# Performance work log

Measured on AMD Instinct MI355X. Metric: run time of the kernel, lower is better.

Reference implementation:

```python
import jax, jax.numpy as jnp
import numpy as np

D_MODEL = 14
N_HEADS = 2
SINK_TEMP = 0.1
SINK_ITERS = 20
EPS = 1e-10


def setup_inputs() -> dict:
    key = jax.random.key(0)
    ks = jax.random.split(key, 12)
    b, n, d = 64, 1024, D_MODEL
    s = 1.0 / np.sqrt(d)
    return {
        "x": jax.random.normal(ks[0], (b, n, d), dtype=jnp.float32),
        "certainty": jax.random.uniform(ks[1], (b, n), dtype=jnp.float32),
        "permutation": jax.random.randint(ks[2], (b, n), 0, n).astype(jnp.int64),
        "Wq": jax.random.normal(ks[3], (d, d), dtype=jnp.float32) * s,
        "bq": jnp.zeros((d,), dtype=jnp.float32),
        "Wk": jax.random.normal(ks[4], (d, d), dtype=jnp.float32) * s,
        "bk": jnp.zeros((d,), dtype=jnp.float32),
        "Wv": jax.random.normal(ks[5], (d, d), dtype=jnp.float32) * s,
        "bv": jnp.zeros((d,), dtype=jnp.float32),
        "Wo": jax.random.normal(ks[6], (d, d), dtype=jnp.float32) * s,
        "bo": jnp.zeros((d,), dtype=jnp.float32),
    }


def _split_heads(t, b, n):
    # (b, n, d) -> (b, H, n, hd)
    return t.reshape(b, n, N_HEADS, D_MODEL // N_HEADS).transpose(0, 2, 1, 3)


def reference(x, certainty, permutation, Wq, bq, Wk, bk, Wv, bv, Wo, bo):
    b, n, d = x.shape
    hd = d // N_HEADS
    Q = _split_heads(x @ Wq.T + bq, b, n)
    K = _split_heads(x @ Wk.T + bk, b, n)
    V = _split_heads(x @ Wv.T + bv, b, n)
    scores = jnp.einsum("bhqd,bhkd->bhqk", Q, K) / jnp.sqrt(jnp.float32(hd))
    attn = jax.nn.softmax(scores, axis=-1)  # dropout is identity at eval
    out = jnp.einsum("bhqk,bhkd->bhqd", attn, V)
    out = out.transpose(0, 2, 1, 3).reshape(b, n, d)
    out = out @ Wo.T + bo

    avg_attn = attn.mean(axis=1)  # (b, n, n)
    entropy = -jnp.sum(avg_attn * jnp.log(avg_attn + EPS), axis=-1)  # (b, n)
    max_entropy = jnp.log(jnp.float32(n))
    cert_update = jax.nn.sigmoid(max_entropy - entropy)
    new_certainty = jnp.maximum(certainty, cert_update)

    logits = jnp.log(avg_attn + EPS)
    P = jnp.exp(logits / SINK_TEMP)

    def body(_, P):
        P = P / (P.sum(axis=-1, keepdims=True) + EPS)
        P = P / (P.sum(axis=-2, keepdims=True) + EPS)
        return P

    P = jax.lax.fori_loop(0, SINK_ITERS, body, P)
    new_perm = jnp.argmax(P, axis=-1)  # (b, n)
    new_permutation = jnp.take_along_axis(permutation, new_perm, axis=1)
    return out, new_certainty, new_permutation
```

## Files before the change

### kernel.cpp

```cpp
#include <hip/hip_runtime.h>

#define EPSF    1e-10f
#define MAXENT  6.93147180559945286f
#define SCALEF  0.37796447300922720f

__device__ __forceinline__ float wave_sum(float v) {
#pragma unroll
  for (int off = 32; off > 0; off >>= 1) v += __shfl_xor(v, off);
  return v;
}
__device__ __forceinline__ void wave_sum2(float& a, float& b) {
#pragma unroll
  for (int off = 32; off > 0; off >>= 1) {
    a += __shfl_xor(a, off);
    b += __shfl_xor(b, off);
  }
}
__device__ __forceinline__ void fma4(float a, float4 b, float4& c) {
  c.x = fmaf(a, b.x, c.x); c.y = fmaf(a, b.y, c.y);
  c.z = fmaf(a, b.z, c.z); c.w = fmaf(a, b.w, c.w);
}
__device__ __forceinline__ float dot4(float4 a, float4 b, float acc) {
  acc = fmaf(a.x, b.x, acc); acc = fmaf(a.y, b.y, acc);
  acc = fmaf(a.z, b.z, acc); acc = fmaf(a.w, b.w, acc);
  return acc;
}
__device__ __forceinline__ float4 exp4(float4 s) {
  return make_float4(__expf(s.x), __expf(s.y), __expf(s.z), __expf(s.w));
}
__device__ __forceinline__ float p0e(float s1, float s2, float E1, float E2) {
  float p = fmaf(E1, __expf(s1), fmaf(E2, __expf(s2), EPSF));
  float p2 = p * p, p4 = p2 * p2, p5 = p4 * p;
  return p5 * p5;
}

__global__ __launch_bounds__(256) void qkv_kernel(
    const float* __restrict__ x,
    const float* __restrict__ Wq, const float* __restrict__ bq,
    const float* __restrict__ Wk, const float* __restrict__ bk,
    const float* __restrict__ Wv, const float* __restrict__ bv,
    float* __restrict__ Qt, float* __restrict__ Kt, float* __restrict__ Vt,
    float* __restrict__ R, float* __restrict__ CA, float* __restrict__ CB) {
  int row = blockIdx.x * 256 + threadIdx.x;
  int b = row >> 10, i = row & 1023;
  float xv[14];
#pragma unroll
  for (int k = 0; k < 14; k++) xv[k] = x[row * 14 + k];
#pragma unroll
  for (int d = 0; d < 14; d++) {
    float q = bq[d], kk = bk[d], vv = bv[d];
#pragma unroll
    for (int k = 0; k < 14; k++) {
      q  = fmaf(xv[k], Wq[d * 14 + k], q);
      kk = fmaf(xv[k], Wk[d * 14 + k], kk);
      vv = fmaf(xv[k], Wv[d * 14 + k], vv);
    }
    int o = b * 14336 + d * 1024 + i;
    Qt[o] = q * SCALEF;
    Kt[o] = kk; Vt[o] = vv;
  }
  R[row] = 1.0f;
  CA[row] = 1.0f;
  CB[row] = 1.0f;
}

__global__ __launch_bounds__(256, 2) void attn_kernel(
    const float* __restrict__ Qt, const float* __restrict__ Kt, const float* __restrict__ Vt,
    const float* __restrict__ cert_in,
    const float* __restrict__ WoG, const float* __restrict__ boG,
    float* __restrict__ E1o, float* __restrict__ E2o,
    float* __restrict__ out_, float* __restrict__ cert_out) {
  __shared__ float4 Kl[3584];
  __shared__ float WoS[196];
  __shared__ float boS[14];
  int b = blockIdx.x >> 7;
  int rg = blockIdx.x & 127;
  int tid = threadIdx.x;
  const float4* Ktb = (const float4*)(Kt + b * 14336);
  for (int idx = tid; idx < 3584; idx += 256) Kl[idx] = Ktb[idx];
  if (tid < 196) WoS[tid] = WoG[tid];
  if (tid < 14) boS[tid] = boG[tid];
  __syncthreads();

  int wave = tid >> 6, lane = tid & 63;
  int i0 = rg * 8 + wave * 2;
  float q0[14], q1[14];
#pragma unroll
  for (int d = 0; d < 14; d++) {
    q0[d] = Qt[b * 14336 + d * 1024 + i0];
    q1[d] = Qt[b * 14336 + d * 1024 + i0 + 1];
  }

  float4 e10[4], e20[4], e11[4], e21[4];
  float L10 = 0.f, L20 = 0.f, L11 = 0.f, L21 = 0.f;
  float acc0[14], acc1[14];
#pragma unroll
  for (int d = 0; d < 14; d++) { acc0[d] = 0.f; acc1[d] = 0.f; }
  const float4* Vtb = (const float4*)(Vt + b * 14336);
#pragma unroll
  for (int t = 0; t < 4; t++) {
    int g = t * 64 + lane;
    float4 kv[7];
#pragma unroll
    for (int d = 0; d < 7; d++) kv[d] = Kl[d * 256 + g];
    float4 sa = {0,0,0,0}, sb = {0,0,0,0};
#pragma unroll
    for (int d = 0; d < 7; d++) { fma4(q0[d], kv[d], sa); fma4(q1[d], kv[d], sb); }
    e10[t] = exp4(sa); e11[t] = exp4(sb);
    L10 += e10[t].x + e10[t].y + e10[t].z + e10[t].w;
    L11 += e11[t].x + e11[t].y + e11[t].z + e11[t].w;
#pragma unroll
    for (int d = 0; d < 7; d++) kv[d] = Kl[(d + 7) * 256 + g];
    sa = make_float4(0,0,0,0); sb = make_float4(0,0,0,0);
#pragma unroll
    for (int d = 0; d < 7; d++) { fma4(q0[d + 7], kv[d], sa); fma4(q1[d + 7], kv[d], sb); }
    e20[t] = exp4(sa); e21[t] = exp4(sb);
    L20 += e20[t].x + e20[t].y + e20[t].z + e20[t].w;
    L21 += e21[t].x + e21[t].y + e21[t].z + e21[t].w;
#pragma unroll
    for (int d = 0; d < 7; d++) {
      float4 vv = Vtb[d * 256 + g];
      acc0[d] += e10[t].x * vv.x + e10[t].y * vv.y + e10[t].z * vv.z + e10[t].w * vv.w;
      acc1[d] += e11[t].x * vv.x + e11[t].y * vv.y + e11[t].z * vv.z + e11[t].w * vv.w;
    }
#pragma unroll
    for (int d = 7; d < 14; d++) {
      float4 vv = Vtb[d * 256 + g];
      acc0[d] += e20[t].x * vv.x + e20[t].y * vv.y + e20[t].z * vv.z + e20[t].w * vv.w;
      acc1[d] += e21[t].x * vv.x + e21[t].y * vv.y + e21[t].z * vv.z + e21[t].w * vv.w;
    }
  }
  wave_sum2(L10, L20); wave_sum2(L11, L21);
  float i10 = 1.0f / L10, i20 = 1.0f / L20, i11 = 1.0f / L11, i21 = 1.0f / L21;

  float ent0 = 0.f, ent1 = 0.f;
#pragma unroll
  for (int t = 0; t < 4; t++) {
    float a;
    a = 0.5f * (e10[t].x * i10 + e20[t].x * i20); ent0 -= a * __logf(a + EPSF);
    a = 0.5f * (e10[t].y * i10 + e20[t].y * i20); ent0 -= a * __logf(a + EPSF);
    a = 0.5f * (e10[t].z * i10 + e20[t].z * i20); ent0 -= a * __logf(a + EPSF);
    a = 0.5f * (e10[t].w * i10 + e20[t].w * i20); ent0 -= a * __logf(a + EPSF);
    a = 0.5f * (e11[t].x * i11 + e21[t].x * i21); ent1 -= a * __logf(a + EPSF);
    a = 0.5f * (e11[t].y * i11 + e21[t].y * i21); ent1 -= a * __logf(a + EPSF);
    a = 0.5f * (e11[t].z * i11 + e21[t].z * i21); ent1 -= a * __logf(a + EPSF);
    a = 0.5f * (e11[t].w * i11 + e21[t].w * i21); ent1 -= a * __logf(a + EPSF);
  }
  wave_sum2(ent0, ent1);
#pragma unroll
  for (int d = 0; d < 14; d += 2) wave_sum2(acc0[d], acc0[d + 1]);
#pragma unroll
  for (int d = 0; d < 14; d += 2) wave_sum2(acc1[d], acc1[d + 1]);

  int row0 = b * 1024 + i0;
  if (lane == 0) {
    E1o[row0] = 0.5f * i10;  E2o[row0] = 0.5f * i20;
    E1o[row0 + 1] = 0.5f * i11; E2o[row0 + 1] = 0.5f * i21;
    cert_out[row0] = fmaxf(cert_in[row0], 1.0f / (1.0f + __expf(ent0 - MAXENT)));
    cert_out[row0 + 1] = fmaxf(cert_in[row0 + 1], 1.0f / (1.0f + __expf(ent1 - MAXENT)));
  }
  if (lane < 14) {
    int d = lane;
    float av0[14], av1[14];
#pragma unroll
    for (int k = 0; k < 14; k++) {
      av0[k] = acc0[k] * (k < 7 ? i10 : i20);
      av1[k] = acc1[k] * (k < 7 ? i11 : i21);
    }
    float s0 = boS[d], s1 = boS[d];
#pragma unroll
    for (int k = 0; k < 14; k++) {
      s0 = fmaf(av0[k], WoS[d * 14 + k], s0);
      s1 = fmaf(av1[k], WoS[d * 14 + k], s1);
    }
    out_[(size_t)row0 * 14 + d] = s0;
    out_[(size_t)(row0 + 1) * 14 + d] = s1;
  }
}


__global__ __launch_bounds__(512) void p0sink1_kernel(
    const float* __restrict__ Qt, const float* __restrict__ Kt,
    const float* __restrict__ E1, const float* __restrict__ E2,
    float* __restrict__ P0, float* __restrict__ R,
    float* __restrict__ vpart, int b0, int G) {
  __shared__ float4 Kl[3584];
  int gb = blockIdx.x >> 5, blk = blockIdx.x & 31;
  int b = b0 + gb;
  int tid = threadIdx.x;
  const float4* Ktb = (const float4*)(Kt + b * 14336);
  for (int idx = tid; idx < 3584; idx += 512) Kl[idx] = Ktb[idx];
  __syncthreads();

  int wave = tid >> 6, lane = tid & 63;
  int i0 = blk * 32 + wave * 4;
  float q[4][14], e1r[4], e2r[4], u[4];
#pragma unroll
  for (int rr = 0; rr < 4; rr++) {
#pragma unroll
    for (int d = 0; d < 14; d++) q[rr][d] = Qt[b * 14336 + d * 1024 + i0 + rr];
    e1r[rr] = E1[b * 1024 + i0 + rr];
    e2r[rr] = E2[b * 1024 + i0 + rr];
    u[rr] = 0.f;
  }
  float4* P0f4 = (float4*)P0;
#pragma unroll
  for (int t = 0; t < 4; t++) {
    int g = t * 64 + lane;
    float4 kv[14];
#pragma unroll
    for (int d = 0; d < 14; d++) kv[d] = Kl[d * 256 + g];
#pragma unroll
    for (int rr = 0; rr < 4; rr++) {
      float4 s1 = {0,0,0,0}, s2 = {0,0,0,0};
#pragma unroll
      for (int d = 0; d < 7; d++)  fma4(q[rr][d], kv[d], s1);
#pragma unroll
      for (int d = 7; d < 14; d++) fma4(q[rr][d], kv[d], s2);
      float4 pv;
      pv.x = p0e(s1.x, s2.x, e1r[rr], e2r[rr]);
      pv.y = p0e(s1.y, s2.y, e1r[rr], e2r[rr]);
      pv.z = p0e(s1.z, s2.z, e1r[rr], e2r[rr]);
      pv.w = p0e(s1.w, s2.w, e1r[rr], e2r[rr]);
      P0f4[(size_t)(gb * 1024 + i0 + rr) * 256 + g] = pv;
      u[rr] += pv.x; u[rr] += pv.y; u[rr] += pv.z; u[rr] += pv.w;
    }
  }
  wave_sum2(u[0], u[1]); wave_sum2(u[2], u[3]);
  float rv[4];
#pragma unroll
  for (int rr = 0; rr < 4; rr++) {
    float r0 = 1.0f;
    rv[rr] = fminf(r0 / fmaf(r0, u[rr], EPSF), 1e37f);
  }
  if (lane == 0) {
#pragma unroll
    for (int rr = 0; rr < 4; rr++) R[b * 1024 + i0 + rr] = rv[rr];
  }
  int l0 = lane, l1 = 64 + lane, l2 = 128 + lane, l3 = 192 + lane;
  float4 v0 = {0,0,0,0}, v1 = {0,0,0,0}, v2 = {0,0,0,0}, v3 = {0,0,0,0};
  const float4* base = P0f4 + (size_t)(gb * 1024 + i0) * 256;
#pragma unroll
  for (int rr = 0; rr < 4; rr++) {
    const float4* row = base + rr * 256;
    float4 a0 = row[l0], a1 = row[l1], a2 = row[l2], a3 = row[l3];
    fma4(rv[rr], a0, v0); fma4(rv[rr], a1, v1); fma4(rv[rr], a2, v2); fma4(rv[rr], a3, v3);
  }
  __syncthreads();
  float* vbuf = (float*)Kl;
  float4* vb4 = (float4*)vbuf;
  vb4[wave * 256 + l0] = v0; vb4[wave * 256 + l1] = v1;
  vb4[wave * 256 + l2] = v2; vb4[wave * 256 + l3] = v3;
  __syncthreads();
  for (int col = tid; col < 1024; col += 512) {
    float v = 0.f;
#pragma unroll
    for (int w = 0; w < 8; w++) v += vbuf[w * 1024 + col];
    vpart[(size_t)(blk * G + gb) * 1024 + col] = v;
  }
}

#define SINK_LOGS 4
#define SINK_S    16
__global__ __launch_bounds__(512) void sink_fused(
    const float* __restrict__ P0, const float* __restrict__ Cin,
    float* __restrict__ Cout, float* __restrict__ R,
    const float* __restrict__ vprev, float* __restrict__ vcur,
    int b0, int G, int Sprev) {
  __shared__ float Cl[1024];
  __shared__ float vbuf[8192];
  int tid = threadIdx.x;
  int gb = blockIdx.x >> SINK_LOGS, slice = blockIdx.x & (SINK_S - 1);
  int b = b0 + gb;

  if (tid < 256) {
    float4 cv = ((const float4*)(Cin + b * 1024))[tid];
    const float4* vp = (const float4*)vprev + (size_t)gb * 256 + tid;
    float4 v = {0, 0, 0, 0};
#pragma unroll 4
    for (int s = 0; s < Sprev; s++) {
      float4 t = vp[(size_t)s * G * 256];
      v.x += t.x; v.y += t.y; v.z += t.z; v.w += t.w;
    }
    cv.x = fminf(cv.x / fmaf(cv.x, v.x, EPSF), 1e37f);
    cv.y = fminf(cv.y / fmaf(cv.y, v.y, EPSF), 1e37f);
    cv.z = fminf(cv.z / fmaf(cv.z, v.z, EPSF), 1e37f);
    cv.w = fminf(cv.w / fmaf(cv.w, v.w, EPSF), 1e37f);
    if (slice == 0) ((float4*)(Cout + b * 1024))[tid] = cv;
    ((float4*)Cl)[tid] = cv;
  }
  __syncthreads();

  int wave = tid >> 6, lane = tid & 63;
  int i0 = slice * 64 + wave * 8;
  int rbase = b * 1024 + i0;
  int l0 = lane, l1 = 64 + lane, l2 = 128 + lane, l3 = 192 + lane;
  const float4* Cl4 = (const float4*)Cl;
  float4 c0 = Cl4[l0], c1 = Cl4[l1], c2 = Cl4[l2], c3 = Cl4[l3];
  float4 v0 = {0,0,0,0}, v1 = {0,0,0,0}, v2 = {0,0,0,0}, v3 = {0,0,0,0};
  const float4* base = (const float4*)P0 + (size_t)(gb * 1024 + i0) * 256;

  float rreg[8];
#pragma unroll
  for (int r = 0; r < 8; r++) rreg[r] = R[rbase + r];

  float4 a0 = base[l0], a1 = base[l1], a2 = base[l2], a3 = base[l3];
  float4 b0f = base[256 + l0], b1f = base[256 + l1], b2f = base[256 + l2], b3f = base[256 + l3];

#pragma unroll
  for (int r = 0; r < 8; r += 2) {
    float4 na0, na1, na2, na3, nb0, nb1, nb2, nb3;
    if (r + 2 < 8) {
      const float4* nxt = base + (r + 2) * 256;
      na0 = nxt[l0]; na1 = nxt[l1]; na2 = nxt[l2]; na3 = nxt[l3];
      nb0 = nxt[256 + l0]; nb1 = nxt[256 + l1]; nb2 = nxt[256 + l2]; nb3 = nxt[256 + l3];
    }
    float ua = dot4(a3, c3, dot4(a2, c2, dot4(a1, c1, dot4(a0, c0, 0.f))));
    float ub = dot4(b3f, c3, dot4(b2f, c2, dot4(b1f, c1, dot4(b0f, c0, 0.f))));
    wave_sum2(ua, ub);
    float rva = rreg[r], rvb = rreg[r + 1];
    rva = fminf(rva / fmaf(rva, ua, EPSF), 1e37f);
    rvb = fminf(rvb / fmaf(rvb, ub, EPSF), 1e37f);
    if (lane == 0) { R[rbase + r] = rva; R[rbase + r + 1] = rvb; }
    fma4(rva, a0, v0); fma4(rva, a1, v1); fma4(rva, a2, v2); fma4(rva, a3, v3);
    fma4(rvb, b0f, v0); fma4(rvb, b1f, v1); fma4(rvb, b2f, v2); fma4(rvb, b3f, v3);
    if (r + 2 < 8) {
      a0 = na0; a1 = na1; a2 = na2; a3 = na3;
      b0f = nb0; b1f = nb1; b2f = nb2; b3f = nb3;
    }
  }
  float4* vb4 = (float4*)vbuf;
  vb4[wave * 256 + l0] = v0; vb4[wave * 256 + l1] = v1;
  vb4[wave * 256 + l2] = v2; vb4[wave * 256 + l3] = v3;
  __syncthreads();
  for (int col = tid; col < 1024; col += 512) {
    float v = 0.f;
#pragma unroll
    for (int w = 0; w < 8; w++) v += vbuf[w * 1024 + col];
    vcur[(size_t)(slice * G + gb) * 1024 + col] = v;
  }
}

__global__ __launch_bounds__(256) void cfinal_kernel(
    const float* __restrict__ Cin, float* __restrict__ Cfin,
    const float* __restrict__ vprev, int b0, int G) {
  int idx = blockIdx.x * 256 + threadIdx.x;
  int gb = idx >> 10, col = idx & 1023;
  const float* vp = vprev + gb * 1024 + col;
  float v = 0.f;
#pragma unroll
  for (int s = 0; s < SINK_S; s++) v += vp[(size_t)s * G * 1024];
  int o = (b0 + gb) * 1024 + col;
  float cv = Cin[o];
  Cfin[o] = fminf(cv / fmaf(cv, v, EPSF), 1e37f);
}

__global__ __launch_bounds__(512) void argmaxP_kernel(
    const float* __restrict__ P0, const float* __restrict__ Cg,
    const int* __restrict__ perm, float* __restrict__ perm_out, int b0) {
  int gb = blockIdx.x >> 7, rg = blockIdx.x & 127;
  int b = b0 + gb;
  int tid = threadIdx.x;
  int wave = tid >> 6, lane = tid & 63;
  int i = rg * 8 + wave;
  const float4* Cb = (const float4*)(Cg + b * 1024);
  const float4* Prow = (const float4*)P0 + (size_t)(gb * 1024 + i) * 256;

  float best = -1.0f;
  int bj = 0;
#pragma unroll
  for (int t = 0; t < 4; t++) {
    int g = t * 64 + lane;
    float4 pv = Prow[g], cv = Cb[g];
    float val;
    val = pv.x * cv.x; if (val > best) { best = val; bj = 4 * g + 0; }
    val = pv.y * cv.y; if (val > best) { best = val; bj = 4 * g + 1; }
    val = pv.z * cv.z; if (val > best) { best = val; bj = 4 * g + 2; }
    val = pv.w * cv.w; if (val > best) { best = val; bj = 4 * g + 3; }
  }
#pragma unroll
  for (int off = 32; off > 0; off >>= 1) {
    float ob = __shfl_xor(best, off);
    int oj = __shfl_xor(bj, off);
    if (ob > best || (ob == best && oj < bj)) { best = ob; bj = oj; }
  }
  if (lane == 0) perm_out[b * 1024 + i] = (float)perm[b * 1024 + bj];
}


__global__ __launch_bounds__(512) void sinkA_kernel(
    const float* __restrict__ Qt, const float* __restrict__ Kt,
    const float* __restrict__ E1, const float* __restrict__ E2,
    const float* __restrict__ C, float* __restrict__ R) {
  __shared__ float4 Kl[3584];
  int b = blockIdx.x >> 5, blk = blockIdx.x & 31;
  int tid = threadIdx.x;
  const float4* Ktb = (const float4*)(Kt + b * 14336);
  for (int idx = tid; idx < 3584; idx += 512) Kl[idx] = Ktb[idx];
  __syncthreads();
  int wave = tid >> 6, lane = tid & 63;
  int i0 = blk * 32 + wave * 4;
  float q[4][14], e1r[4], e2r[4], u[4];
#pragma unroll
  for (int rr = 0; rr < 4; rr++) {
#pragma unroll
    for (int d = 0; d < 14; d++) q[rr][d] = Qt[b * 14336 + d * 1024 + i0 + rr];
    e1r[rr] = E1[b * 1024 + i0 + rr];
    e2r[rr] = E2[b * 1024 + i0 + rr];
    u[rr] = 0.f;
  }
  const float4* Cb = (const float4*)(C + b * 1024);
#pragma unroll
  for (int t = 0; t < 4; t++) {
    int g = t * 64 + lane;
    float4 kv[14];
#pragma unroll
    for (int d = 0; d < 14; d++) kv[d] = Kl[d * 256 + g];
    float4 cv = Cb[g];
#pragma unroll
    for (int rr = 0; rr < 4; rr++) {
      float4 s1 = {0,0,0,0}, s2 = {0,0,0,0};
#pragma unroll
      for (int d = 0; d < 7; d++)  fma4(q[rr][d], kv[d], s1);
#pragma unroll
      for (int d = 7; d < 14; d++) fma4(q[rr][d], kv[d], s2);
      u[rr] += p0e(s1.x, s2.x, e1r[rr], e2r[rr]) * cv.x;
      u[rr] += p0e(s1.y, s2.y, e1r[rr], e2r[rr]) * cv.y;
      u[rr] += p0e(s1.z, s2.z, e1r[rr], e2r[rr]) * cv.z;
      u[rr] += p0e(s1.w, s2.w, e1r[rr], e2r[rr]) * cv.w;
    }
  }
#pragma unroll
  for (int rr = 0; rr < 4; rr++) u[rr] = wave_sum(u[rr]);
  if (lane == 0) {
#pragma unroll
    for (int rr = 0; rr < 4; rr++) {
      int o = b * 1024 + i0 + rr;
      float rv = R[o];
      R[o] = fminf(rv / fmaf(rv, u[rr], EPSF), 1e37f);
    }
  }
}

__global__ __launch_bounds__(512) void sinkB_kernel(
    const float* __restrict__ Qt, const float* __restrict__ Kt,
    const float* __restrict__ E1, const float* __restrict__ E2,
    const float* __restrict__ R, float* __restrict__ C) {
  __shared__ float4 Ql[3584];
  int b = blockIdx.x >> 5, blk = blockIdx.x & 31;
  int tid = threadIdx.x;
  const float4* Qtb = (const float4*)(Qt + b * 14336);
  for (int idx = tid; idx < 3584; idx += 512) Ql[idx] = Qtb[idx];
  __syncthreads();
  int wave = tid >> 6, lane = tid & 63;
  int j0 = blk * 32 + wave * 4;
  float kk[4][14], v[4];
#pragma unroll
  for (int rr = 0; rr < 4; rr++) {
#pragma unroll
    for (int d = 0; d < 14; d++) kk[rr][d] = Kt[b * 14336 + d * 1024 + j0 + rr];
    v[rr] = 0.f;
  }
  const float4* E1b = (const float4*)(E1 + b * 1024);
  const float4* E2b = (const float4*)(E2 + b * 1024);
  const float4* Rb  = (const float4*)(R + b * 1024);
#pragma unroll
  for (int t = 0; t < 4; t++) {
    int g = t * 64 + lane;
    float4 qv[14];
#pragma unroll
    for (int d = 0; d < 14; d++) qv[d] = Ql[d * 256 + g];
    float4 e1v = E1b[g], e2v = E2b[g], rv = Rb[g];
#pragma unroll
    for (int rr = 0; rr < 4; rr++) {
      float4 s1 = {0,0,0,0}, s2 = {0,0,0,0};
#pragma unroll
      for (int d = 0; d < 7; d++)  fma4(kk[rr][d], qv[d], s1);
#pragma unroll
      for (int d = 7; d < 14; d++) fma4(kk[rr][d], qv[d], s2);
      v[rr] += p0e(s1.x, s2.x, e1v.x, e2v.x) * rv.x;
      v[rr] += p0e(s1.y, s2.y, e1v.y, e2v.y) * rv.y;
      v[rr] += p0e(s1.z, s2.z, e1v.z, e2v.z) * rv.z;
      v[rr] += p0e(s1.w, s2.w, e1v.w, e2v.w) * rv.w;
    }
  }
#pragma unroll
  for (int rr = 0; rr < 4; rr++) v[rr] = wave_sum(v[rr]);
  if (lane == 0) {
#pragma unroll
    for (int rr = 0; rr < 4; rr++) {
      int o = b * 1024 + j0 + rr;
      float cv = C[o];
      C[o] = fminf(cv / fmaf(cv, v[rr], EPSF), 1e37f);
    }
  }
}

__global__ __launch_bounds__(512) void argmax_kernel(
    const float* __restrict__ Qt, const float* __restrict__ Kt,
    const float* __restrict__ E1, const float* __restrict__ E2,
    const float* __restrict__ C, const int* __restrict__ perm,
    float* __restrict__ perm_out) {
  __shared__ float4 Kl[3584];
  int b = blockIdx.x >> 7, rg = blockIdx.x & 127;
  int tid = threadIdx.x;
  const float4* Ktb = (const float4*)(Kt + b * 14336);
  for (int idx = tid; idx < 3584; idx += 512) Kl[idx] = Ktb[idx];
  __syncthreads();
  int wave = tid >> 6, lane = tid & 63;
  int i = rg * 8 + wave;
  int row = b * 1024 + i;
  float q[14];
#pragma unroll
  for (int d = 0; d < 14; d++) q[d] = Qt[b * 14336 + d * 1024 + i];
  float e1r = E1[row], e2r = E2[row];
  const float4* Cb = (const float4*)(C + b * 1024);
  float best = -1.0f;
  int bj = 0;
#pragma unroll
  for (int t = 0; t < 4; t++) {
    int g = t * 64 + lane;
    float4 kv[14];
#pragma unroll
    for (int d = 0; d < 14; d++) kv[d] = Kl[d * 256 + g];
    float4 cv = Cb[g];
    float4 s1 = {0,0,0,0}, s2 = {0,0,0,0};
#pragma unroll
    for (int d = 0; d < 7; d++)  fma4(q[d], kv[d], s1);
#pragma unroll
    for (int d = 7; d < 14; d++) fma4(q[d], kv[d], s2);
    float val;
    val = p0e(s1.x, s2.x, e1r, e2r) * cv.x; if (val > best) { best = val; bj = 4 * g + 0; }
    val = p0e(s1.y, s2.y, e1r, e2r) * cv.y; if (val > best) { best = val; bj = 4 * g + 1; }
    val = p0e(s1.z, s2.z, e1r, e2r) * cv.z; if (val > best) { best = val; bj = 4 * g + 2; }
    val = p0e(s1.w, s2.w, e1r, e2r) * cv.w; if (val > best) { best = val; bj = 4 * g + 3; }
  }
#pragma unroll
  for (int off = 32; off > 0; off >>= 1) {
    float ob = __shfl_xor(best, off);
    int oj = __shfl_xor(bj, off);
    if (ob > best || (ob == best && oj < bj)) { best = ob; bj = oj; }
  }
  if (lane == 0) perm_out[row] = (float)perm[b * 1024 + bj];
}

extern "C" void kernel_launch(void* const* d_in, const int* in_sizes, int n_in,
                              void* d_out, int out_size, void* d_ws, size_t ws_size,
                              hipStream_t stream) {
  const float* x    = (const float*)d_in[0];
  const float* cert = (const float*)d_in[1];
  const int*   perm = (const int*)d_in[2];
  const float* Wq = (const float*)d_in[3];
  const float* bq = (const float*)d_in[4];
  const float* Wk = (const float*)d_in[5];
  const float* bk = (const float*)d_in[6];
  const float* Wv = (const float*)d_in[7];
  const float* bv = (const float*)d_in[8];
  const float* Wo = (const float*)d_in[9];
  const float* bo = (const float*)d_in[10];

  float* out      = (float*)d_out;
  float* cert_out = out + 917504;
  float* perm_out = out + 983040;

  float* ws = (float*)d_ws;
  float* Qt = ws;
  float* Kt = Qt + 917504;
  float* Vt = Kt + 917504;
  float* E1 = Vt + 917504;
  float* E2 = E1 + 65536;
  float* R  = E2 + 65536;
  float* CA = R + 65536;
  float* CB = CA + 65536;
  float* vpp0 = CB + 65536;

  size_t base_f = 3080192u;
  size_t avail_f = (ws_size / 4 > base_f) ? (ws_size / 4 - base_f) : 0;
  size_t perG = 2u * 32 * 1024 + 1048576u;
  int G = 0;
  if (avail_f >= 64 * perG) G = 64;
  else if (avail_f >= 32 * perG) G = 32;
  else if (avail_f >= 16 * perG) G = 16;

  float* Cbuf[2] = {CA, CB};

  qkv_kernel<<<256, 256, 0, stream>>>(x, Wq, bq, Wk, bk, Wv, bv, Qt, Kt, Vt, R, CA, CB);
  attn_kernel<<<8192, 256, 0, stream>>>(Qt, Kt, Vt, cert, Wo, bo, E1, E2, out, cert_out);

  if (G >= 16) {
    float* vpp[2] = {vpp0, vpp0 + (size_t)32 * G * 1024};
    float* P0 = vpp0 + (size_t)2 * 32 * G * 1024;
    for (int b0 = 0; b0 < 64; b0 += G) {
      p0sink1_kernel<<<G * 32, 512, 0, stream>>>(Qt, Kt, E1, E2, P0, R, vpp[1], b0, G);
      for (int it = 2; it <= 20; it++) {
        const float* vprev = vpp[(it - 1) & 1];
        float* vcur = vpp[it & 1];
        const float* Cin = Cbuf[it & 1];
        float* Cout = Cbuf[(it + 1) & 1];
        int Sprev = (it == 2) ? 32 : 16;
        sink_fused<<<G * SINK_S, 512, 0, stream>>>(P0, Cin, Cout, R, vprev, vcur, b0, G, Sprev);
      }
      cfinal_kernel<<<G * 4, 256, 0, stream>>>(Cbuf[1], Cbuf[0], vpp[0], b0, G);
      argmaxP_kernel<<<G * 128, 512, 0, stream>>>(P0, Cbuf[0], perm, perm_out, b0);
    }
  } else {
    for (int it = 0; it < 20; it++) {
      sinkA_kernel<<<2048, 512, 0, stream>>>(Qt, Kt, E1, E2, CA, R);
      sinkB_kernel<<<2048, 512, 0, stream>>>(Qt, Kt, E1, E2, R, CA);
    }
    argmax_kernel<<<8192, 512, 0, stream>>>(Qt, Kt, E1, E2, CA, perm, perm_out);
  }
}
```

Baseline: 1.423 ms.

## Fuse Sinkhorn iterations into one cooperative kernel with grid sync

Replaces the 19 per-iteration sink_fused launches plus the cfinal and argmax kernels with a single cooperative kernel. It keeps the row scales in registers across iterations and uses grid-wide sync between them, and it software-prefetches P rows two at a time. The aim is to remove launch overhead and the inter-kernel gaps across iterations. In exchange it depends on all G*16 blocks being co-resident, checked through an occupancy query, and it adds grid-sync costs. The perm type is cast to int here, which may not match the caller.

```diff
diff --git a/kernel.cpp b/kernel.cpp
--- a/kernel.cpp
+++ b/kernel.cpp
@@ -1,4 +1,7 @@
 #include <hip/hip_runtime.h>
+#include <hip/hip_cooperative_groups.h>
+
+namespace cg = cooperative_groups;
 
 #define EPSF    1e-10f
 #define MAXENT  6.93147180559945286f
@@ -260,6 +263,136 @@
   }
 }
 
+__global__ __launch_bounds__(512, 4) void sink_coop(
+    const float* __restrict__ P0, float* __restrict__ CA, float* __restrict__ CB,
+    const float* __restrict__ R,
+    float* __restrict__ vppA, float* __restrict__ vppB,
+    const int* __restrict__ perm, float* __restrict__ perm_out,
+    int b0, int G) {
+  cg::grid_group gridg = cg::this_grid();
+  __shared__ float Cl[1024];
+  __shared__ float vbuf[8192];
+  int tid = threadIdx.x;
+  int gb = blockIdx.x >> 4, slice = blockIdx.x & 15;
+  int b = b0 + gb;
+  int wave = tid >> 6, lane = tid & 63;
+  int i0 = slice * 64 + wave * 8;
+  int l0 = lane, l1 = 64 + lane, l2 = 128 + lane, l3 = 192 + lane;
+  const float4* base = (const float4*)P0 + (size_t)(gb * 1024 + i0) * 256;
+
+  float rreg[8];
+#pragma unroll
+  for (int r = 0; r < 8; r++) rreg[r] = R[b * 1024 + i0 + r];
+
+  for (int it = 2; it <= 20; it++) {
+    const float* vprev = (it & 1) ? vppA : vppB;
+    float* vcur = (it & 1) ? vppB : vppA;
+    const float* Cin = (it & 1) ? CB : CA;
+    float* Cout = (it & 1) ? CA : CB;
+    int Sprev = (it == 2) ? 32 : 16;
+
+    if (tid < 256) {
+      float4 cv = ((const float4*)(Cin + b * 1024))[tid];
+      const float4* vp = (const float4*)vprev + (size_t)gb * 256 + tid;
+      float4 v = {0, 0, 0, 0};
+#pragma unroll 4
+      for (int s = 0; s < Sprev; s++) {
+        float4 t = vp[(size_t)s * G * 256];
+        v.x += t.x; v.y += t.y; v.z += t.z; v.w += t.w;
+      }
+      cv.x = fminf(cv.x / fmaf(cv.x, v.x, EPSF), 1e37f);
+      cv.y = fminf(cv.y / fmaf(cv.y, v.y, EPSF), 1e37f);
+      cv.z = fminf(cv.z / fmaf(cv.z, v.z, EPSF), 1e37f);
+      cv.w = fminf(cv.w / fmaf(cv.w, v.w, EPSF), 1e37f);
+      if (slice == 0) ((float4*)(Cout + b * 1024))[tid] = cv;
+      ((float4*)Cl)[tid] = cv;
+    }
+    __syncthreads();
+
+    const float4* Cl4 = (const float4*)Cl;
+    float4 c0 = Cl4[l0], c1 = Cl4[l1], c2 = Cl4[l2], c3 = Cl4[l3];
+    float4 v0 = {0,0,0,0}, v1 = {0,0,0,0}, v2 = {0,0,0,0}, v3 = {0,0,0,0};
+
+    float4 a0 = base[l0], a1 = base[l1], a2 = base[l2], a3 = base[l3];
+    float4 b0f = base[256 + l0], b1f = base[256 + l1], b2f = base[256 + l2], b3f = base[256 + l3];
+
+#pragma unroll
+    for (int r = 0; r < 8; r += 2) {
+      float4 na0, na1, na2, na3, nb0, nb1, nb2, nb3;
+      if (r + 2 < 8) {
+        const float4* nxt = base + (r + 2) * 256;
+        na0 = nxt[l0]; na1 = nxt[l1]; na2 = nxt[l2]; na3 = nxt[l3];
+        nb0 = nxt[256 + l0]; nb1 = nxt[256 + l1]; nb2 = nxt[256 + l2]; nb3 = nxt[256 + l3];
+      }
+      float ua = dot4(a3, c3, dot4(a2, c2, dot4(a1, c1, dot4(a0, c0, 0.f))));
+      float ub = dot4(b3f, c3, dot4(b2f, c2, dot4(b1f, c1, dot4(b0f, c0, 0.f))));
+      wave_sum2(ua, ub);
+      float rva = rreg[r], rvb = rreg[r + 1];
+      rva = fminf(rva / fmaf(rva, ua, EPSF), 1e37f);
+      rvb = fminf(rvb / fmaf(rvb, ub, EPSF), 1e37f);
+      rreg[r] = rva; rreg[r + 1] = rvb;
+      fma4(rva, a0, v0); fma4(rva, a1, v1); fma4(rva, a2, v2); fma4(rva, a3, v3);
+      fma4(rvb, b0f, v0); fma4(rvb, b1f, v1); fma4(rvb, b2f, v2); fma4(rvb, b3f, v3);
+      if (r + 2 < 8) {
+        a0 = na0; a1 = na1; a2 = na2; a3 = na3;
+        b0f = nb0; b1f = nb1; b2f = nb2; b3f = nb3;
+      }
+    }
+    float4* vb4 = (float4*)vbuf;
+    vb4[wave * 256 + l0] = v0; vb4[wave * 256 + l1] = v1;
+    vb4[wave * 256 + l2] = v2; vb4[wave * 256 + l3] = v3;
+    __syncthreads();
+    for (int col = tid; col < 1024; col += 512) {
+      float v = 0.f;
+#pragma unroll
+      for (int w = 0; w < 8; w++) v += vbuf[w * 1024 + col];
+      vcur[(size_t)(slice * G + gb) * 1024 + col] = v;
+    }
+    __threadfence();
+    gridg.sync();
+  }
+
+  if (tid < 256) {
+    float4 cv = ((const float4*)(CB + b * 1024))[tid];
+    const float4* vp = (const float4*)vppA + (size_t)gb * 256 + tid;
+    float4 v = {0, 0, 0, 0};
+#pragma unroll
+    for (int s = 0; s < 16; s++) {
+      float4 t = vp[(size_t)s * G * 256];
+      v.x += t.x; v.y += t.y; v.z += t.z; v.w += t.w;
+    }
+    cv.x = fminf(cv.x / fmaf(cv.x, v.x, EPSF), 1e37f);
+    cv.y = fminf(cv.y / fmaf(cv.y, v.y, EPSF), 1e37f);
+    cv.z = fminf(cv.z / fmaf(cv.z, v.z, EPSF), 1e37f);
+    cv.w = fminf(cv.w / fmaf(cv.w, v.w, EPSF), 1e37f);
+    ((float4*)Cl)[tid] = cv;
+  }
+  __syncthreads();
+  const float4* Cl4 = (const float4*)Cl;
+  for (int r = 0; r < 8; r++) {
+    const float4* Prow = base + r * 256;
+    float best = -1.0f;
+    int bj = 0;
+#pragma unroll
+    for (int t = 0; t < 4; t++) {
+      int g = t * 64 + lane;
+      float4 pv = Prow[g], cv = Cl4[g];
+      float val;
+      val = pv.x * cv.x; if (val > best) { best = val; bj = 4 * g + 0; }
+      val = pv.y * cv.y; if (val > best) { best = val; bj = 4 * g + 1; }
+      val = pv.z * cv.z; if (val > best) { best = val; bj = 4 * g + 2; }
+      val = pv.w * cv.w; if (val > best) { best = val; bj = 4 * g + 3; }
+    }
+#pragma unroll
+    for (int off = 32; off > 0; off >>= 1) {
+      float ob = __shfl_xor(best, off);
+      int oj = __shfl_xor(bj, off);
+      if (ob > best || (ob == best && oj < bj)) { best = ob; bj = oj; }
+    }
+    if (lane == 0) perm_out[b * 1024 + i0 + r] = (float)perm[b * 1024 + bj];
+  }
+}
+
 #define SINK_LOGS 4
 #define SINK_S    16
 __global__ __launch_bounds__(512) void sink_fused(
@@ -582,26 +715,45 @@
   else if (avail_f >= 32 * perG) G = 32;
   else if (avail_f >= 16 * perG) G = 16;
 
-  float* Cbuf[2] = {CA, CB};
-
   qkv_kernel<<<256, 256, 0, stream>>>(x, Wq, bq, Wk, bk, Wv, bv, Qt, Kt, Vt, R, CA, CB);
   attn_kernel<<<8192, 256, 0, stream>>>(Qt, Kt, Vt, cert, Wo, bo, E1, E2, out, cert_out);
 
   if (G >= 16) {
-    float* vpp[2] = {vpp0, vpp0 + (size_t)32 * G * 1024};
+    float* vppA = vpp0;
+    float* vppB = vpp0 + (size_t)32 * G * 1024;
     float* P0 = vpp0 + (size_t)2 * 32 * G * 1024;
+
+    int maxB = 0;
+    bool coop_ok = (hipOccupancyMaxActiveBlocksPerMultiprocessor(&maxB, sink_coop, 512, 0)
+                    == hipSuccess) && (maxB * 256 >= G * 16);
+
     for (int b0 = 0; b0 < 64; b0 += G) {
-      p0sink1_kernel<<<G * 32, 512, 0, stream>>>(Qt, Kt, E1, E2, P0, R, vpp[1], b0, G);
-      for (int it = 2; it <= 20; it++) {
-        const float* vprev = vpp[(it - 1) & 1];
-        float* vcur = vpp[it & 1];
-        const float* Cin = Cbuf[it & 1];
-        float* Cout = Cbuf[(it + 1) & 1];
-        int Sprev = (it == 2) ? 32 : 16;
-        sink_fused<<<G * SINK_S, 512, 0, stream>>>(P0, Cin, Cout, R, vprev, vcur, b0, G, Sprev);
+      p0sink1_kernel<<<G * 32, 512, 0, stream>>>(Qt, Kt, E1, E2, P0, R, vppB, b0, G);
+      if (coop_ok) {
+        const float* P0c = P0;
+        const int* permc = perm;
+        int b0v = b0, Gv = G;
+        float *CAp = CA, *CBp = CB, *vA = vppA, *vB = vppB, *po = perm_out;
+        const float* Rc = R;
+        void* args[] = {(void*)&P0c, (void*)&CAp, (void*)&CBp, (void*)&Rc,
+                        (void*)&vA, (void*)&vB, (void*)&permc, (void*)&po,
+                        (void*)&b0v, (void*)&Gv};
+        hipLaunchCooperativeKernel((void*)sink_coop, dim3(G * 16), dim3(512),
+                                   args, 0, stream);
+      } else {
+        float* Cbuf[2] = {CA, CB};
+        float* vpp[2] = {vppA, vppB};
+        for (int it = 2; it <= 20; it++) {
+          const float* vprev = vpp[(it - 1) & 1];
+          float* vcur = vpp[it & 1];
+          const float* Cin = Cbuf[it & 1];
+          float* Cout = Cbuf[(it + 1) & 1];
+          int Sprev = (it == 2) ? 32 : 16;
+          sink_fused<<<G * SINK_S, 512, 0, stream>>>(P0, Cin, Cout, R, vprev, vcur, b0, G, Sprev);
+        }
+        cfinal_kernel<<<G * 4, 256, 0, stream>>>(Cbuf[1], Cbuf[0], vpp[0], b0, G);
+        argmaxP_kernel<<<G * 128, 512, 0, stream>>>(P0, Cbuf[0], perm, perm_out, b0);
       }
-      cfinal_kernel<<<G * 4, 256, 0, stream>>>(Cbuf[1], Cbuf[0], vpp[0], b0, G);
-      argmaxP_kernel<<<G * 128, 512, 0, stream>>>(P0, Cbuf[0], perm, perm_out, b0);
     }
   } else {
     for (int it = 0; it < 20; it++) {
```

Measured after the change: 1.446 ms. No clear change (+1.6%).
